# Kernel optimization log

Hardware: AMD Instinct MI355X
Metric: run time of the kernel (lower is better)

## Reference

```python
import jax, jax.numpy as jnp
import numpy as np

B, N, PD, LAT, H, STEPS = 32, 2048, 2, 128, 256, 5
DIN = PD + 1 + LAT  # [x, t, context]


def setup_inputs() -> dict:
    key = jax.random.key(0)
    ks = jax.random.split(key, 8)
    def lin(k, dout, din):
        # He-ish init scaled down to keep tanh unsaturated (matches torch default scale-wise)
        return jax.random.normal(k, (dout, din), jnp.float32) / np.float32(np.sqrt(din))
    return {
        "x": jax.random.normal(ks[0], (B, N, PD), jnp.float32),
        "z": jax.random.normal(ks[1], (B, LAT), jnp.float32),
        "W1": lin(ks[2], H, DIN),
        "b1": jnp.zeros((H,), jnp.float32),
        "W2": lin(ks[3], H, H),
        "b2": jnp.zeros((H,), jnp.float32),
        "W3": lin(ks[4], PD, H),
        "b3": jnp.zeros((PD,), jnp.float32),
        "out_scale": jnp.ones((1,), jnp.float32),  # self.output_scale
    }


def _vel_and_div(xp, ctx, t, W1, b1, W2, b2, W3, b3, out_scale):
    """Velocity v = net([x, t, ctx]) * scale and exact divergence d v_i / d x_i.

    The MLP acts pointwise, so the Jacobian w.r.t. x is a per-point 2x2 matrix;
    its trace is computed analytically via tangent propagation through the tanh
    layers (replaces the per-dim torch.autograd.grad loop).
    """
    tvec = jnp.ones(xp.shape[:-1] + (1,), xp.dtype) * t
    u = jnp.concatenate([xp, tvec, ctx], axis=-1)          # [B,N,DIN]
    h1 = jnp.tanh(u @ W1.T + b1)                            # [B,N,H]
    h2 = jnp.tanh(h1 @ W2.T + b2)                           # [B,N,H]
    v = (h2 @ W3.T + b3) * out_scale                        # [B,N,PD]
    g1 = 1.0 - h1 * h1
    g2 = 1.0 - h2 * h2
    div = jnp.zeros(xp.shape[:-1], xp.dtype)
    for i in range(PD):  # fixed tiny loop over point_dim=2
        dh1 = g1 * W1[:, i]            # tangent through layer 1, basis e_i
        dh2 = g2 * (dh1 @ W2.T)        # tangent through layer 2
        div = div + (dh2 @ W3[i]) * out_scale[0]
    return v, div[..., None]           # [B,N,PD], [B,N,1]


def reference(x, z, W1, b1, W2, b2, W3, b3, out_scale):
    """Faithful translation of StablePointFlow2DVAE.cnf_forward's executed
    (log-det) Euler loop: per-step velocity + exact-trace divergence; note the
    context also accumulates div*dt (broadcast), exactly as the torch code's
    `s + d[:, :, :s.shape[-1]] * dt` does. Returns (y, log_det)."""
    Bx, Nx = x.shape[0], x.shape[1]
    ctx0 = jnp.broadcast_to(z[:, None, :], (Bx, Nx, z.shape[-1]))
    dt = jnp.asarray(1.0 / STEPS, x.dtype)
    ts = jnp.arange(STEPS, dtype=x.dtype) * dt

    def step(carry, t):
        xs, ctx, ld = carry
        v, div = _vel_and_div(xs, ctx, t, W1, b1, W2, b2, W3, b3, out_scale)
        return (xs + v * dt, ctx + div * dt, ld + div * dt), None

    ld0 = jnp.zeros((Bx, Nx, 1), x.dtype)
    (y, _, log_det), _ = jax.lax.scan(step, (x, ctx0, ld0), ts)
    return y, log_det
```

## Files before the change

### kernel.cpp

```cpp
#include <hip/hip_runtime.h>

#define NPTS 65536
#define HH 256
#define DIN 131
#define LAT 128
#define STEPS 5
#define DT 0.2f
#define P 32

typedef unsigned int uint;
typedef unsigned short ushort;
typedef __attribute__((ext_vector_type(8))) short short8;
typedef __attribute__((ext_vector_type(4))) float floatx4;

__device__ __forceinline__ float tanh_fast(float x) {
    float e = __builtin_amdgcn_exp2f(x * 2.8853900817779268f);
    return 1.0f - 2.0f * __builtin_amdgcn_rcpf(e + 1.0f);
}

__device__ __forceinline__ ushort f2bf(float f) {
    uint u = __builtin_bit_cast(uint, f);
    u += 0x7fffu + ((u >> 16) & 1u);
    return (ushort)(u >> 16);
}

__device__ __forceinline__ uint cvt_pk_bf16(float lo, float hi) {
    uint r;
    asm("v_cvt_pk_bf16_f32 %0, %1, %2" : "=v"(r) : "v"(lo), "v"(hi));
    return r;
}

__device__ __forceinline__ float dpp_sum16(float x) {
    int t;
    t = __builtin_amdgcn_update_dpp(0, __builtin_bit_cast(int, x), 0x111, 0xf, 0xf, true);
    x += __builtin_bit_cast(float, t);
    t = __builtin_amdgcn_update_dpp(0, __builtin_bit_cast(int, x), 0x112, 0xf, 0xf, true);
    x += __builtin_bit_cast(float, t);
    t = __builtin_amdgcn_update_dpp(0, __builtin_bit_cast(int, x), 0x114, 0xf, 0xf, true);
    x += __builtin_bit_cast(float, t);
    t = __builtin_amdgcn_update_dpp(0, __builtin_bit_cast(int, x), 0x118, 0xf, 0xf, true);
    x += __builtin_bit_cast(float, t);
    return x;
}

__global__ void prep_kernel(const float* __restrict__ z, const float* __restrict__ W1,
                            const float* __restrict__ b1, const float* __restrict__ W2,
                            float* __restrict__ a1, float* __restrict__ rsv,
                            ushort* __restrict__ wsw)
{
    int tid = blockIdx.x * 256 + threadIdx.x;
    if (tid < 8192) {
        int b = tid >> 8, h = tid & 255;
        const float* wrow = W1 + h * DIN;
        const float* zb = z + b * LAT;
        float s = b1[h], r = 0.f;
        for (int l = 0; l < LAT; ++l) { float wv = wrow[3 + l]; s += wv * zb[l]; r += wv; }
        a1[tid] = s;
        if (b == 0) rsv[h] = r;
    } else {
        int t = tid - 8192;
        int lane = t & 63, kt = (t >> 6) & 7, nt = t >> 9;
        int n = nt * 16 + (lane & 15);
        int k = kt * 32 + (lane >> 4) * 8;
        const float* src = W2 + n * HH + k;
        ushort* dst = wsw + t * 8;
        #pragma unroll
        for (int j = 0; j < 8; ++j) dst[j] = f2bf(src[j]);
    }
}

__global__ __launch_bounds__(256, 2) void cnf_kernel(
        const float* __restrict__ xin, const float* __restrict__ W1,
        const float* __restrict__ b2, const float* __restrict__ W3,
        const float* __restrict__ b3, const float* __restrict__ osc,
        const float* __restrict__ a1, const float* __restrict__ rsv,
        const ushort* __restrict__ wsw, float* __restrict__ out)
{
    __shared__ __align__(16) ushort Vb[3 * P * HH];
    __shared__ __align__(16) float4 XC[P];

    const int tid = threadIdx.x;
    const int lane = tid & 63;
    const int w = tid >> 6;
    const int r15 = lane & 15;
    const int q = lane >> 4;
    const int blk = blockIdx.x;
    const int b = blk >> 6;
    const int pbase = blk * P;
    const int hp = tid & 127;
    const int h0 = hp * 2;
    const int pst = tid >> 7;

    const float wa  = W1[h0 * DIN + 0],  wbv = W1[(h0 + 1) * DIN + 0];
    const float wc  = W1[h0 * DIN + 1],  wd  = W1[(h0 + 1) * DIN + 1];
    const float wta = W1[h0 * DIN + 2],  wtb = W1[(h0 + 1) * DIN + 2];
    const float ra  = rsv[h0],           rb  = rsv[h0 + 1];
    float ba = a1[b * HH + h0];
    float bb = a1[b * HH + h0 + 1];

    if (tid < P) {
        int gp = pbase + tid;
        XC[tid] = (float4){xin[gp * 2 + 0], xin[gp * 2 + 1], 0.f, 0.f};
    }
    const float osdt = osc[0] * DT;
    const float ab0 = (w == 0) ? b3[0] * osdt : 0.f;
    const float ab1 = (w == 0) ? b3[1] * osdt : 0.f;
    float w30r[4], w31r[4], b2r[4];
    #pragma unroll
    for (int n = 0; n < 4; ++n) {
        int j = (w * 4 + n) * 16 + r15;
        w30r[n] = W3[j];
        w31r[n] = W3[HH + j];
        b2r[n] = b2[j];
    }
    __syncthreads();

    const char* vrow = (const char*)Vb + r15 * 512;
    const int xr = (r15 & 7) << 4;

    for (int s = 0; s < STEPS; ++s) {
        #pragma unroll 8
        for (int i = 0; i < 16; ++i) {
            int p = pst + 2 * i;
            float4 xc = XC[p];
            float pa = ba + wa  * xc.x + wc * xc.y + ra * xc.z;
            float pb = bb + wbv * xc.x + wd * xc.y + rb * xc.z;
            float ha = tanh_fast(pa), hb = tanh_fast(pb);
            float ga = 1.f - ha * ha, gb = 1.f - hb * hb;
            char* dst = (char*)Vb + p * 512 + ((4 * hp) ^ ((p & 7) << 4));
            *(uint*)(dst)         = cvt_pk_bf16(ha,       hb);
            *(uint*)(dst + 16384) = cvt_pk_bf16(ga * wa,  gb * wbv);
            *(uint*)(dst + 32768) = cvt_pk_bf16(ga * wc,  gb * wd);
        }
        ba += wta * DT;
        bb += wtb * DT;
        __syncthreads();

        floatx4 acc[3][2][4];
        #pragma unroll
        for (int v = 0; v < 3; ++v)
            #pragma unroll
            for (int mt = 0; mt < 2; ++mt)
                #pragma unroll
                for (int n = 0; n < 4; ++n)
                    acc[v][mt][n] = (floatx4){0.f, 0.f, 0.f, 0.f};

        const ushort* wb_ = wsw + (size_t)(w * 4) * 4096 + (size_t)lane * 8;

        __builtin_amdgcn_s_setprio(1);
        #pragma unroll
        for (int kt = 0; kt < 8; ++kt) {
            const int boff = (kt * 64 + q * 16) ^ xr;
            const char* ap = vrow + boff;
            short8 af[3][2];
            #pragma unroll
            for (int v = 0; v < 3; ++v)
                #pragma unroll
                for (int mt = 0; mt < 2; ++mt)
                    af[v][mt] = *(const short8*)(ap + v * 16384 + mt * 8192);
            #pragma unroll
            for (int n = 0; n < 4; ++n) {
                short8 bfr = *(const short8*)(wb_ + (size_t)(n * 8 + kt) * 512);
                #pragma unroll
                for (int mt = 0; mt < 2; ++mt)
                    #pragma unroll
                    for (int v = 0; v < 3; ++v)
                        acc[v][mt][n] = __builtin_amdgcn_mfma_f32_16x16x32_bf16(
                            af[v][mt], bfr, acc[v][mt][n], 0, 0, 0);
            }
        }
        __builtin_amdgcn_s_setprio(0);

        #pragma unroll
        for (int mt = 0; mt < 2; ++mt) {
            float sv0[4] = {0,0,0,0}, sv1[4] = {0,0,0,0}, sdv[4] = {0,0,0,0};
            #pragma unroll
            for (int n = 0; n < 4; ++n) {
                const float w0 = w30r[n], w1 = w31r[n], bbj = b2r[n];
                #pragma unroll
                for (int r = 0; r < 4; ++r) {
                    float h2 = tanh_fast(acc[0][mt][n][r] + bbj);
                    float g2 = 1.f - h2 * h2;
                    sv0[r] += h2 * w0;
                    sv1[r] += h2 * w1;
                    sdv[r] += g2 * (acc[1][mt][n][r] * w0 + acc[2][mt][n][r] * w1);
                }
            }
            #pragma unroll
            for (int r = 0; r < 4; ++r) {
                float ta = dpp_sum16(sv0[r]);
                float tb = dpp_sum16(sv1[r]);
                float td = dpp_sum16(sdv[r]);
                if (r15 == 15) {
                    int p = mt * 16 + q * 4 + r;
                    atomicAdd(&XC[p].x, ta * osdt + ab0);
                    atomicAdd(&XC[p].y, tb * osdt + ab1);
                    atomicAdd(&XC[p].z, td * osdt);
                }
            }
        }
        __syncthreads();
    }

    if (tid < P) {
        int gp = pbase + tid;
        float4 xc = XC[tid];
        out[gp * 2 + 0] = xc.x;
        out[gp * 2 + 1] = xc.y;
        out[NPTS * 2 + gp] = xc.z;
    }
}

extern "C" void kernel_launch(void* const* d_in, const int* in_sizes, int n_in,
                              void* d_out, int out_size, void* d_ws, size_t ws_size,
                              hipStream_t stream) {
    const float* x   = (const float*)d_in[0];
    const float* z   = (const float*)d_in[1];
    const float* W1  = (const float*)d_in[2];
    const float* b1  = (const float*)d_in[3];
    const float* W2  = (const float*)d_in[4];
    const float* b2  = (const float*)d_in[5];
    const float* W3  = (const float*)d_in[6];
    const float* b3  = (const float*)d_in[7];
    const float* osc = (const float*)d_in[8];

    float* a1  = (float*)d_ws;
    float* rsv = (float*)((char*)d_ws + 32768);
    ushort* wsw = (ushort*)((char*)d_ws + 33792);

    hipLaunchKernelGGL(prep_kernel, dim3(64), dim3(256), 0, stream, z, W1, b1, W2, a1, rsv, wsw);
    hipLaunchKernelGGL(cnf_kernel, dim3(2048), dim3(256), 0, stream,
                       x, W1, b2, W3, b3, osc, a1, rsv, wsw, (float*)d_out);
}
```

Before: 222.6 us.

## Ping-pong point halves to overlap layer-1 tanh with MFMA of other half

Splits the 32 points per block into two groups of 16 and alternates between them over 10 half-steps. While one group's layer-2 MFMA results are reduced, the layer-1 tanh/tangent tiles for the other group's next step are written into LDS. This aims to hide the VALU-heavy layer-1 work behind matrix work and halves the accumulator register footprint. In exchange, the W2 fragments are reloaded from global/L2 twice as often, and each barrier phase covers less work.

```diff
diff --git a/kernel.cpp b/kernel.cpp
--- a/kernel.cpp
+++ b/kernel.cpp
@@ -95,8 +95,8 @@
     const float wc  = W1[h0 * DIN + 1],  wd  = W1[(h0 + 1) * DIN + 1];
     const float wta = W1[h0 * DIN + 2],  wtb = W1[(h0 + 1) * DIN + 2];
     const float ra  = rsv[h0],           rb  = rsv[h0 + 1];
-    float ba = a1[b * HH + h0];
-    float bb = a1[b * HH + h0 + 1];
+    const float ba  = a1[b * HH + h0];
+    const float bb  = a1[b * HH + h0 + 1];
 
     if (tid < P) {
         int gp = pbase + tid;
@@ -117,73 +117,85 @@
 
     const char* vrow = (const char*)Vb + r15 * 512;
     const int xr = (r15 & 7) << 4;
-
-    for (int s = 0; s < STEPS; ++s) {
-        #pragma unroll 8
-        for (int i = 0; i < 16; ++i) {
-            int p = pst + 2 * i;
-            float4 xc = XC[p];
-            float pa = ba + wa  * xc.x + wc * xc.y + ra * xc.z;
-            float pb = bb + wbv * xc.x + wd * xc.y + rb * xc.z;
-            float ha = tanh_fast(pa), hb = tanh_fast(pb);
-            float ga = 1.f - ha * ha, gb = 1.f - hb * hb;
-            char* dst = (char*)Vb + p * 512 + ((4 * hp) ^ ((p & 7) << 4));
-            *(uint*)(dst)         = cvt_pk_bf16(ha,       hb);
-            *(uint*)(dst + 16384) = cvt_pk_bf16(ga * wa,  gb * wbv);
-            *(uint*)(dst + 32768) = cvt_pk_bf16(ga * wc,  gb * wd);
-        }
-        ba += wta * DT;
-        bb += wtb * DT;
-        __syncthreads();
-
-        floatx4 acc[3][2][4];
+    const ushort* wb_ = wsw + (size_t)(w * 4) * 4096 + (size_t)lane * 8;
+
+    #pragma unroll
+    for (int i = 0; i < 8; ++i) {
+        int p = pst + 2 * i;
+        float4 xc = XC[p];
+        float pa = ba + wa  * xc.x + wc * xc.y + ra * xc.z;
+        float pb = bb + wbv * xc.x + wd * xc.y + rb * xc.z;
+        float ha = tanh_fast(pa), hb = tanh_fast(pb);
+        float ga = 1.f - ha * ha, gb = 1.f - hb * hb;
+        char* dst = (char*)Vb + p * 512 + ((4 * hp) ^ ((p & 7) << 4));
+        *(uint*)(dst)         = cvt_pk_bf16(ha,       hb);
+        *(uint*)(dst + 16384) = cvt_pk_bf16(ga * wa,  gb * wbv);
+        *(uint*)(dst + 32768) = cvt_pk_bf16(ga * wc,  gb * wd);
+    }
+    __syncthreads();
+
+    for (int k = 0; k < 10; ++k) {
+        const int g = k & 1;
+        const char* ap_base = vrow + g * 8192;
+
+        floatx4 acc[3][4];
         #pragma unroll
         for (int v = 0; v < 3; ++v)
             #pragma unroll
-            for (int mt = 0; mt < 2; ++mt)
-                #pragma unroll
-                for (int n = 0; n < 4; ++n)
-                    acc[v][mt][n] = (floatx4){0.f, 0.f, 0.f, 0.f};
-
-        const ushort* wb_ = wsw + (size_t)(w * 4) * 4096 + (size_t)lane * 8;
+            for (int n = 0; n < 4; ++n)
+                acc[v][n] = (floatx4){0.f, 0.f, 0.f, 0.f};
 
         __builtin_amdgcn_s_setprio(1);
         #pragma unroll
         for (int kt = 0; kt < 8; ++kt) {
             const int boff = (kt * 64 + q * 16) ^ xr;
-            const char* ap = vrow + boff;
-            short8 af[3][2];
-            #pragma unroll
-            for (int v = 0; v < 3; ++v)
-                #pragma unroll
-                for (int mt = 0; mt < 2; ++mt)
-                    af[v][mt] = *(const short8*)(ap + v * 16384 + mt * 8192);
+            const char* ap = ap_base + boff;
+            short8 a0f = *(const short8*)(ap);
+            short8 a1f = *(const short8*)(ap + 16384);
+            short8 a2f = *(const short8*)(ap + 32768);
             #pragma unroll
             for (int n = 0; n < 4; ++n) {
                 short8 bfr = *(const short8*)(wb_ + (size_t)(n * 8 + kt) * 512);
-                #pragma unroll
-                for (int mt = 0; mt < 2; ++mt)
-                    #pragma unroll
-                    for (int v = 0; v < 3; ++v)
-                        acc[v][mt][n] = __builtin_amdgcn_mfma_f32_16x16x32_bf16(
-                            af[v][mt], bfr, acc[v][mt][n], 0, 0, 0);
+                acc[0][n] = __builtin_amdgcn_mfma_f32_16x16x32_bf16(a0f, bfr, acc[0][n], 0, 0, 0);
+                acc[1][n] = __builtin_amdgcn_mfma_f32_16x16x32_bf16(a1f, bfr, acc[1][n], 0, 0, 0);
+                acc[2][n] = __builtin_amdgcn_mfma_f32_16x16x32_bf16(a2f, bfr, acc[2][n], 0, 0, 0);
             }
         }
         __builtin_amdgcn_s_setprio(0);
 
-        #pragma unroll
-        for (int mt = 0; mt < 2; ++mt) {
+        if (k < 9) {
+            const int sp = (k + 1) >> 1;
+            const float fs = (float)sp * DT;
+            const float pba = ba + wta * fs;
+            const float pbb = bb + wtb * fs;
+            const int pb0 = (g ^ 1) * 16;
+            #pragma unroll
+            for (int i = 0; i < 8; ++i) {
+                int p = pb0 + pst + 2 * i;
+                float4 xc = XC[p];
+                float pa = pba + wa  * xc.x + wc * xc.y + ra * xc.z;
+                float pb = pbb + wbv * xc.x + wd * xc.y + rb * xc.z;
+                float ha = tanh_fast(pa), hb = tanh_fast(pb);
+                float ga = 1.f - ha * ha, gb = 1.f - hb * hb;
+                char* dst = (char*)Vb + p * 512 + ((4 * hp) ^ ((p & 7) << 4));
+                *(uint*)(dst)         = cvt_pk_bf16(ha,       hb);
+                *(uint*)(dst + 16384) = cvt_pk_bf16(ga * wa,  gb * wbv);
+                *(uint*)(dst + 32768) = cvt_pk_bf16(ga * wc,  gb * wd);
+            }
+        }
+
+        {
             float sv0[4] = {0,0,0,0}, sv1[4] = {0,0,0,0}, sdv[4] = {0,0,0,0};
             #pragma unroll
             for (int n = 0; n < 4; ++n) {
                 const float w0 = w30r[n], w1 = w31r[n], bbj = b2r[n];
                 #pragma unroll
                 for (int r = 0; r < 4; ++r) {
-                    float h2 = tanh_fast(acc[0][mt][n][r] + bbj);
+                    float h2 = tanh_fast(acc[0][n][r] + bbj);
                     float g2 = 1.f - h2 * h2;
                     sv0[r] += h2 * w0;
                     sv1[r] += h2 * w1;
-                    sdv[r] += g2 * (acc[1][mt][n][r] * w0 + acc[2][mt][n][r] * w1);
+                    sdv[r] += g2 * (acc[1][n][r] * w0 + acc[2][n][r] * w1);
                 }
             }
             #pragma unroll
@@ -192,7 +204,7 @@
                 float tb = dpp_sum16(sv1[r]);
                 float td = dpp_sum16(sdv[r]);
                 if (r15 == 15) {
-                    int p = mt * 16 + q * 4 + r;
+                    int p = g * 16 + q * 4 + r;
                     atomicAdd(&XC[p].x, ta * osdt + ab0);
                     atomicAdd(&XC[p].y, tb * osdt + ab1);
                     atomicAdd(&XC[p].z, td * osdt);
```

Measured after the change: 229.1 us. 2.9% more time.

## Stage W2 in LDS and give each wave independent 16-point ownership

Applied to the files above, without the earlier changes.

The whole bf16-swizzled W2, a per-step layer-1 coefficient table and W3/b2 are copied into dynamic LDS once per block. Each wave now owns 16 points end to end. It builds the layer-1 activations and tangents directly in registers as MFMA A-fragments, and it reduces the per-point sums through a small per-wave LDS slot instead of shared atomics. This removes the block-wide barriers each step and the repeated global/L2 reads of W2. In exchange it needs 160KB of LDS per block, which limits occupancy to one 512-thread block per CU, and each wave reads all of W2 from LDS every step.

```diff
diff --git a/kernel.cpp b/kernel.cpp
--- a/kernel.cpp
+++ b/kernel.cpp
@@ -6,12 +6,17 @@
 #define LAT 128
 #define STEPS 5
 #define DT 0.2f
-#define P 32
 
 typedef unsigned int uint;
 typedef unsigned short ushort;
 typedef __attribute__((ext_vector_type(8))) short short8;
 typedef __attribute__((ext_vector_type(4))) float floatx4;
+typedef __attribute__((ext_vector_type(4))) uint uintx4;
+
+#define OFF_W1TAB 131072
+#define OFF_W3    154112
+#define OFF_RED   158208
+#define LDS_TOTAL 160256
 
 __device__ __forceinline__ float tanh_fast(float x) {
     float e = __builtin_amdgcn_exp2f(x * 2.8853900817779268f);
@@ -69,15 +74,14 @@
     }
 }
 
-__global__ __launch_bounds__(256, 2) void cnf_kernel(
+__global__ __launch_bounds__(512, 2) void cnf_kernel(
         const float* __restrict__ xin, const float* __restrict__ W1,
         const float* __restrict__ b2, const float* __restrict__ W3,
         const float* __restrict__ b3, const float* __restrict__ osc,
         const float* __restrict__ a1, const float* __restrict__ rsv,
         const ushort* __restrict__ wsw, float* __restrict__ out)
 {
-    __shared__ __align__(16) ushort Vb[3 * P * HH];
-    __shared__ __align__(16) float4 XC[P];
+    extern __shared__ __align__(16) char sm[];
 
     const int tid = threadIdx.x;
     const int lane = tid & 63;
@@ -85,129 +89,122 @@
     const int r15 = lane & 15;
     const int q = lane >> 4;
     const int blk = blockIdx.x;
-    const int b = blk >> 6;
-    const int pbase = blk * P;
-    const int hp = tid & 127;
-    const int h0 = hp * 2;
-    const int pst = tid >> 7;
-
-    const float wa  = W1[h0 * DIN + 0],  wbv = W1[(h0 + 1) * DIN + 0];
-    const float wc  = W1[h0 * DIN + 1],  wd  = W1[(h0 + 1) * DIN + 1];
-    const float wta = W1[h0 * DIN + 2],  wtb = W1[(h0 + 1) * DIN + 2];
-    const float ra  = rsv[h0],           rb  = rsv[h0 + 1];
-    float ba = a1[b * HH + h0];
-    float bb = a1[b * HH + h0 + 1];
-
-    if (tid < P) {
-        int gp = pbase + tid;
-        XC[tid] = (float4){xin[gp * 2 + 0], xin[gp * 2 + 1], 0.f, 0.f};
-    }
+    const int b = blk >> 4;
+
+    {
+        uintx4* dst = (uintx4*)sm;
+        const uintx4* src = (const uintx4*)wsw;
+        #pragma unroll
+        for (int i = 0; i < 16; ++i) dst[tid + i * 512] = src[tid + i * 512];
+    }
+    if (tid < HH) {
+        const int h = tid;
+        const int kt = h >> 5, rem = h & 31, qq = rem >> 3, u = rem & 7;
+        const float wa = W1[h * DIN + 0];
+        const float wc = W1[h * DIN + 1];
+        const float wt = W1[h * DIN + 2];
+        const float ra = rsv[h];
+        const float ba = a1[b * HH + h];
+        #pragma unroll
+        for (int s = 0; s < STEPS; ++s) {
+            float* rec = (float*)(sm + OFF_W1TAB + s * 4608 + kt * 576 + qq * 144 + u * 16);
+            rec[0] = wa; rec[1] = wc; rec[2] = ra; rec[3] = ba + wt * ((float)s * DT);
+        }
+        float* w3r = (float*)(sm + OFF_W3 + h * 16);
+        w3r[0] = W3[h]; w3r[1] = W3[HH + h]; w3r[2] = b2[h]; w3r[3] = 0.f;
+    }
+
+    const int gp = blk * 128 + w * 16 + r15;
+    float x0 = xin[gp * 2 + 0];
+    float x1 = xin[gp * 2 + 1];
+    float cc = 0.f;
     const float osdt = osc[0] * DT;
-    const float ab0 = (w == 0) ? b3[0] * osdt : 0.f;
-    const float ab1 = (w == 0) ? b3[1] * osdt : 0.f;
-    float w30r[4], w31r[4], b2r[4];
-    #pragma unroll
-    for (int n = 0; n < 4; ++n) {
-        int j = (w * 4 + n) * 16 + r15;
-        w30r[n] = W3[j];
-        w31r[n] = W3[HH + j];
-        b2r[n] = b2[j];
-    }
+    const float b30 = b3[0], b31 = b3[1];
+
     __syncthreads();
 
-    const char* vrow = (const char*)Vb + r15 * 512;
-    const int xr = (r15 & 7) << 4;
+    const char* wtab  = sm + OFF_W1TAB + q * 144;
+    const char* bbase = sm + (size_t)lane * 16;
+    float4* red = (float4*)(sm + OFF_RED) + w * 16;
 
     for (int s = 0; s < STEPS; ++s) {
-        #pragma unroll 8
-        for (int i = 0; i < 16; ++i) {
-            int p = pst + 2 * i;
-            float4 xc = XC[p];
-            float pa = ba + wa  * xc.x + wc * xc.y + ra * xc.z;
-            float pb = bb + wbv * xc.x + wd * xc.y + rb * xc.z;
-            float ha = tanh_fast(pa), hb = tanh_fast(pb);
-            float ga = 1.f - ha * ha, gb = 1.f - hb * hb;
-            char* dst = (char*)Vb + p * 512 + ((4 * hp) ^ ((p & 7) << 4));
-            *(uint*)(dst)         = cvt_pk_bf16(ha,       hb);
-            *(uint*)(dst + 16384) = cvt_pk_bf16(ga * wa,  gb * wbv);
-            *(uint*)(dst + 32768) = cvt_pk_bf16(ga * wc,  gb * wd);
-        }
-        ba += wta * DT;
-        bb += wtb * DT;
-        __syncthreads();
-
-        floatx4 acc[3][2][4];
-        #pragma unroll
-        for (int v = 0; v < 3; ++v)
-            #pragma unroll
-            for (int mt = 0; mt < 2; ++mt)
+        short8 A0[8], A1[8], A2[8];
+        const char* stab = wtab + s * 4608;
+        #pragma unroll
+        for (int kt = 0; kt < 8; ++kt) {
+            const char* kr = stab + kt * 576;
+            uint p0[4], p1[4], p2[4];
+            #pragma unroll
+            for (int up = 0; up < 4; ++up) {
+                const float4 cA = *(const float4*)(kr + up * 32);
+                const float4 cB = *(const float4*)(kr + up * 32 + 16);
+                float pa = cA.w + cA.x * x0 + cA.y * x1 + cA.z * cc;
+                float pb = cB.w + cB.x * x0 + cB.y * x1 + cB.z * cc;
+                float ha = tanh_fast(pa), hb = tanh_fast(pb);
+                float ga = 1.f - ha * ha, gb = 1.f - hb * hb;
+                p0[up] = cvt_pk_bf16(ha, hb);
+                p1[up] = cvt_pk_bf16(ga * cA.x, gb * cB.x);
+                p2[up] = cvt_pk_bf16(ga * cA.y, gb * cB.y);
+            }
+            A0[kt] = __builtin_bit_cast(short8, (uintx4){p0[0], p0[1], p0[2], p0[3]});
+            A1[kt] = __builtin_bit_cast(short8, (uintx4){p1[0], p1[1], p1[2], p1[3]});
+            A2[kt] = __builtin_bit_cast(short8, (uintx4){p2[0], p2[1], p2[2], p2[3]});
+        }
+
+        float sv0[4] = {0,0,0,0}, sv1[4] = {0,0,0,0}, sdv[4] = {0,0,0,0};
+        #pragma unroll
+        for (int pass = 0; pass < 4; ++pass) {
+            floatx4 acc0[4], acc1[4], acc2[4];
+            #pragma unroll
+            for (int n2 = 0; n2 < 4; ++n2) {
+                acc0[n2] = (floatx4){0.f, 0.f, 0.f, 0.f};
+                acc1[n2] = (floatx4){0.f, 0.f, 0.f, 0.f};
+                acc2[n2] = (floatx4){0.f, 0.f, 0.f, 0.f};
+            }
+            #pragma unroll
+            for (int kt = 0; kt < 8; ++kt) {
                 #pragma unroll
-                for (int n = 0; n < 4; ++n)
-                    acc[v][mt][n] = (floatx4){0.f, 0.f, 0.f, 0.f};
-
-        const ushort* wb_ = wsw + (size_t)(w * 4) * 4096 + (size_t)lane * 8;
-
-        __builtin_amdgcn_s_setprio(1);
-        #pragma unroll
-        for (int kt = 0; kt < 8; ++kt) {
-            const int boff = (kt * 64 + q * 16) ^ xr;
-            const char* ap = vrow + boff;
-            short8 af[3][2];
-            #pragma unroll
-            for (int v = 0; v < 3; ++v)
-                #pragma unroll
-                for (int mt = 0; mt < 2; ++mt)
-                    af[v][mt] = *(const short8*)(ap + v * 16384 + mt * 8192);
-            #pragma unroll
-            for (int n = 0; n < 4; ++n) {
-                short8 bfr = *(const short8*)(wb_ + (size_t)(n * 8 + kt) * 512);
-                #pragma unroll
-                for (int mt = 0; mt < 2; ++mt)
-                    #pragma unroll
-                    for (int v = 0; v < 3; ++v)
-                        acc[v][mt][n] = __builtin_amdgcn_mfma_f32_16x16x32_bf16(
-                            af[v][mt], bfr, acc[v][mt][n], 0, 0, 0);
-            }
-        }
-        __builtin_amdgcn_s_setprio(0);
-
-        #pragma unroll
-        for (int mt = 0; mt < 2; ++mt) {
-            float sv0[4] = {0,0,0,0}, sv1[4] = {0,0,0,0}, sdv[4] = {0,0,0,0};
-            #pragma unroll
-            for (int n = 0; n < 4; ++n) {
-                const float w0 = w30r[n], w1 = w31r[n], bbj = b2r[n];
+                for (int n2 = 0; n2 < 4; ++n2) {
+                    const int nt = pass * 4 + n2;
+                    short8 bf = *(const short8*)(bbase + (size_t)(nt * 8 + kt) * 1024);
+                    acc0[n2] = __builtin_amdgcn_mfma_f32_16x16x32_bf16(A0[kt], bf, acc0[n2], 0, 0, 0);
+                    acc1[n2] = __builtin_amdgcn_mfma_f32_16x16x32_bf16(A1[kt], bf, acc1[n2], 0, 0, 0);
+                    acc2[n2] = __builtin_amdgcn_mfma_f32_16x16x32_bf16(A2[kt], bf, acc2[n2], 0, 0, 0);
+                }
+            }
+            #pragma unroll
+            for (int n2 = 0; n2 < 4; ++n2) {
+                const int j = (pass * 4 + n2) * 16 + r15;
+                const float4 w3c = *(const float4*)(sm + OFF_W3 + j * 16);
                 #pragma unroll
                 for (int r = 0; r < 4; ++r) {
-                    float h2 = tanh_fast(acc[0][mt][n][r] + bbj);
+                    float h2 = tanh_fast(acc0[n2][r] + w3c.z);
                     float g2 = 1.f - h2 * h2;
-                    sv0[r] += h2 * w0;
-                    sv1[r] += h2 * w1;
-                    sdv[r] += g2 * (acc[1][mt][n][r] * w0 + acc[2][mt][n][r] * w1);
+                    sv0[r] += h2 * w3c.x;
+                    sv1[r] += h2 * w3c.y;
+                    sdv[r] += g2 * (acc1[n2][r] * w3c.x + acc2[n2][r] * w3c.y);
                 }
             }
-            #pragma unroll
-            for (int r = 0; r < 4; ++r) {
-                float ta = dpp_sum16(sv0[r]);
-                float tb = dpp_sum16(sv1[r]);
-                float td = dpp_sum16(sdv[r]);
-                if (r15 == 15) {
-                    int p = mt * 16 + q * 4 + r;
-                    atomicAdd(&XC[p].x, ta * osdt + ab0);
-                    atomicAdd(&XC[p].y, tb * osdt + ab1);
-                    atomicAdd(&XC[p].z, td * osdt);
-                }
-            }
-        }
-        __syncthreads();
-    }
-
-    if (tid < P) {
-        int gp = pbase + tid;
-        float4 xc = XC[tid];
-        out[gp * 2 + 0] = xc.x;
-        out[gp * 2 + 1] = xc.y;
-        out[NPTS * 2 + gp] = xc.z;
+        }
+
+        #pragma unroll
+        for (int r = 0; r < 4; ++r) {
+            float ta = dpp_sum16(sv0[r]);
+            float tb = dpp_sum16(sv1[r]);
+            float td = dpp_sum16(sdv[r]);
+            if (r15 == 15) red[q * 4 + r] = (float4){ta, tb, td, 0.f};
+        }
+        __threadfence_block();
+        const float4 rd = red[r15];
+        x0 += (rd.x + b30) * osdt;
+        x1 += (rd.y + b31) * osdt;
+        cc += rd.z * osdt;
+    }
+
+    if (q == 0) {
+        out[gp * 2 + 0] = x0;
+        out[gp * 2 + 1] = x1;
+        out[NPTS * 2 + gp] = cc;
     }
 }
 
@@ -228,7 +225,14 @@
     float* rsv = (float*)((char*)d_ws + 32768);
     ushort* wsw = (ushort*)((char*)d_ws + 33792);
 
+    static bool attr_set = false;
+    if (!attr_set) {
+        hipFuncSetAttribute((const void*)cnf_kernel,
+                            hipFuncAttributeMaxDynamicSharedMemorySize, LDS_TOTAL);
+        attr_set = true;
+    }
+
     hipLaunchKernelGGL(prep_kernel, dim3(64), dim3(256), 0, stream, z, W1, b1, W2, a1, rsv, wsw);
-    hipLaunchKernelGGL(cnf_kernel, dim3(2048), dim3(256), 0, stream,
+    hipLaunchKernelGGL(cnf_kernel, dim3(512), dim3(512), LDS_TOTAL, stream,
                        x, W1, b2, W3, b3, osc, a1, rsv, wsw, (float*)d_out);
 }
```

Result: slower. 287.5 us (+29.2%).
